# Performance work log

Measured on AMD Instinct MI355X. Metric: run time of the kernel, lower is better.

Reference implementation:

```python
import jax, jax.numpy as jnp
import numpy as np

B, S, NH, HID, NL = 64, 512, 16, 512, 16
W_WIN, PAD, THR, BW = 5, 2, 5.0, 0.1
D_IN = 1 + 2 * NH


def setup_inputs():
    key = jax.random.key(0)
    ks = jax.random.split(key, 16)
    time = jax.random.uniform(ks[0], (B, S)) * 1000.0
    mag = 15.0 + jax.random.normal(ks[1], (B, S))
    err = 0.01 + 0.1 * jax.random.uniform(ks[2], (B, S))
    sc = 0.05
    p = {}
    p["light_curve"] = jnp.stack([time, mag, err], axis=1)  # (B,3,S)
    p["valid_mask"] = jnp.ones((B, S), dtype=bool)
    p["frequency"] = 0.5 + 4.5 * jax.random.uniform(ks[3], (B,))
    p["W_ih0"] = sc * jax.random.normal(ks[4], (3 * HID, D_IN))
    p["b_ih0"] = jnp.zeros((3 * HID,))
    p["W_hh0"] = sc * jax.random.normal(ks[5], (3 * HID, HID))
    p["b_hh0"] = jnp.zeros((3 * HID,))
    p["W_ih1"] = sc * jax.random.normal(ks[6], (3 * HID, HID))
    p["b_ih1"] = jnp.zeros((3 * HID,))
    p["W_hh1"] = sc * jax.random.normal(ks[7], (3 * HID, HID))
    p["b_hh1"] = jnp.zeros((3 * HID,))
    p["Wl1"] = sc * jax.random.normal(ks[8], (HID, HID))
    p["bl1"] = jnp.zeros((HID,))
    p["Wl2"] = sc * jax.random.normal(ks[9], (NL, HID))
    p["bl2"] = jnp.zeros((NL,))
    return p


def _flag_outliers(phase, mag):
    # Sorted-window weighted (Epanechnikov in circular phase-delta) mean/std outlier test.
    # Caller guarantees all points valid (setup uses an all-True mask), so index_select == identity.
    perm = jnp.argsort(phase)
    ps, ms = phase[perm], mag[perm]

    def windows(x):
        xp = jnp.concatenate([x[-PAD:], x, x[:PAD]])  # circular pad
        return jnp.stack([xp[i:i + S] for i in range(W_WIN)], axis=-1)  # (S, w)

    wp, wm = windows(ps), windows(ms)
    cols = jnp.array([i for i in range(W_WIN) if i != PAD])
    dphi = wp[:, cols] - wp[:, PAD:PAD + 1]
    dphi = jnp.remainder(dphi - 0.5, 1.0) - 0.5
    wgt = 0.75 * (1.0 - dphi ** 2)
    wmm = wm[:, cols]
    wsum = wgt.sum(-1)
    loc = (wmm * wgt).sum(-1) / wsum
    scale = jnp.sqrt((((wmm - loc[:, None]) ** 2) * wgt).sum(-1) / (wsum - 1.0))
    thr = loc + THR * scale
    sigma = jnp.zeros_like(mag).at[perm].set(thr)  # inverse-permute (index_copy_)
    return mag > sigma


def _gru_layer(x, W_ih, b_ih, W_hh, b_hh):
    # torch nn.GRU cell math; x: (B,S,D) -> (B,S,H)
    xW = jnp.einsum('bsd,gd->bsg', x, W_ih) + b_ih  # (B,S,3H)

    def step(h, xt):
        hW = h @ W_hh.T + b_hh
        xr, xz, xn = jnp.split(xt, 3, axis=-1)
        hr, hz, hn = jnp.split(hW, 3, axis=-1)
        r = jax.nn.sigmoid(xr + hr)
        z = jax.nn.sigmoid(xz + hz)
        n = jnp.tanh(xn + r * hn)
        h = (1.0 - z) * n + z * h
        return h, h

    h0 = jnp.zeros((x.shape[0], W_hh.shape[1]), x.dtype)
    _, hs = jax.lax.scan(step, h0, jnp.swapaxes(xW, 0, 1))
    return jnp.swapaxes(hs, 0, 1)


def reference(light_curve, valid_mask, frequency, W_ih0, b_ih0, W_hh0, b_hh0,
              W_ih1, b_ih1, W_hh1, b_hh1, Wl1, bl1, Wl2, bl2):
    time, mag, err = light_curve[:, 0], light_curve[:, 1], light_curve[:, 2]
    period = 2.0 / frequency[:, None]  # fold_with_double_period=True (default)
    phase = jnp.remainder(time, period) / period
    outlier = jax.vmap(_flag_outliers)(phase, mag)
    is_valid = valid_mask & ~outlier

    # periodic-kernel interpolation on 50-point grid; align phase to brightness max
    grid = jnp.linspace(0.0, 1.0, 50)
    delta = grid[None, :, None] - phase[:, None, :]  # (B,50,S)
    K = jnp.exp((jnp.cos(2.0 * jnp.pi * delta) - 1.0) / BW ** 2)
    Wk = is_valid[:, None, :].astype(K.dtype) * K
    Wk = Wk / Wk.sum(-1, keepdims=True)
    smooth = (Wk * mag[:, None, :]).sum(-1)  # (B,50)
    phase = phase - grid[jnp.argmax(smooth, axis=-1)][:, None]

    # sort by phase, invalid points last; scaler=None -> loc 0, scale 1
    big = jnp.finfo(jnp.float32).max
    idx = jnp.argsort(jnp.where(is_valid, phase, big), axis=-1)
    phase = jnp.take_along_axis(phase, idx, -1)
    mag = jnp.take_along_axis(mag, idx, -1)
    is_valid = jnp.take_along_axis(is_valid, idx, -1)

    # Fourier phase embedding [cos_1..cos_H, sin_1..sin_H] + mag -> (B,S,2H+1)
    k = jnp.arange(1, NH + 1, dtype=phase.dtype)
    ang = 2.0 * jnp.pi * phase[:, :, None] * k
    emb = jnp.concatenate([jnp.cos(ang), jnp.sin(ang), mag[:, :, None]], axis=-1)

    ht = _gru_layer(emb, W_ih0, b_ih0, W_hh0, b_hh0)
    ht = _gru_layer(ht, W_ih1, b_ih1, W_hh1, b_hh1)

    m = is_valid[:, :, None].astype(ht.dtype)  # context='average'
    ctx = (ht * m).sum(1) / m.sum(1)
    h1 = jax.nn.gelu(ctx @ Wl1.T + bl1, approximate=False)
    z = h1 @ Wl2.T + bl2
    return z
```

## Files before the change

### kernel.cpp

```cpp
#include <hip/hip_runtime.h>


typedef unsigned short u16;
typedef unsigned int u32;
typedef unsigned long long u64;

__device__ __forceinline__ float b2f(u16 u) { return __uint_as_float(((u32)u) << 16); }
__device__ __forceinline__ float blo(u32 u) { return __uint_as_float(u << 16); }
__device__ __forceinline__ float bhi(u32 u) { return __uint_as_float(u & 0xffff0000u); }
__device__ __forceinline__ u16 f2b(float f) {
    u32 x = __float_as_uint(f);
    u32 r = x + 0x7fffu + ((x >> 16) & 1u);
    return (u16)(r >> 16);
}

#define SS 512
#define TWO_PI 6.28318530717958647692f
#define BIGF 3.402823466e+38f
#define PANEL_ELEMS (1536 * 512)
#define FLAGS_BYTES 32768
#define FL(g, f) (((g) * 16 + (f)) * 16)
#define F_A 0
#define F_B 2
#define F_C 4
#define G_A 6
#define G_B 8
#define G_C 10
#define F_PRE 12
#define F_CTX 14

struct P {
    const void* lc;
    const void* freq;
    const void* W[12];
    void* out;
    void* ws;
    unsigned long long ws_size;
};

__device__ __forceinline__ bool inputs_are_bf16(const void* freq) {
    const u16* q = (const u16*)freq;
    bool ok = true;
    for (int i = 0; i < 64; ++i) {
        float v = b2f(q[i]);
        ok = ok && (v >= 0.4f) && (v <= 5.5f);
    }
    return ok;
}

template<bool BF>
__device__ __forceinline__ float ldw(const void* p, size_t i) {
    if constexpr (BF) return b2f(((const u16*)p)[i]);
    else              return ((const float*)p)[i];
}
template<bool BF>
__device__ __forceinline__ const void* rowp(const void* base, int row) {
    if constexpr (BF) return (const void*)((const u16*)base + (size_t)row * 512);
    else              return (const void*)((const float*)base + (size_t)row * 512);
}

__device__ __forceinline__ void sc_store_f(float* ptr, float v) {
    __hip_atomic_store(ptr, v, __ATOMIC_RELAXED, __HIP_MEMORY_SCOPE_AGENT);
}
__device__ __forceinline__ float sc_load_f(const float* ptr) {
    return __hip_atomic_load(ptr, __ATOMIC_RELAXED, __HIP_MEMORY_SCOPE_AGENT);
}
__device__ __forceinline__ void sc_store_i(int* ptr, int v) {
    __hip_atomic_store(ptr, v, __ATOMIC_RELAXED, __HIP_MEMORY_SCOPE_AGENT);
}
__device__ __forceinline__ int sc_load_i(const int* ptr) {
    return __hip_atomic_load(ptr, __ATOMIC_RELAXED, __HIP_MEMORY_SCOPE_AGENT);
}
__device__ __forceinline__ void waitge(const int* f, int v, int* dead) {
    if (*dead) return;
    int it = 0;
    while (sc_load_i(f) < v) {
        __builtin_amdgcn_s_sleep(1);
        if (++it > 2000000) { *dead = 1; break; }
    }
}

template<bool BF>
__device__ void build_panel_one(const void* W, int tid, char* panbase) {
    if constexpr (BF) {
        const uint4* Ws = (const uint4*)W;
        uint4* panel = (uint4*)panbase;
        for (int i = tid; i < 1536 * 64; i += 512) {
            int r = i >> 6, k8 = i & 63;
            panel[(size_t)k8 * 1536 + r] = Ws[i];
        }
    } else {
        const float4* Ws = (const float4*)W;
        float4* panel = (float4*)panbase;
        for (int i = tid; i < 1536 * 128; i += 512) {
            int r = i >> 7, k4 = i & 127;
            panel[(size_t)k4 * 1536 + r] = Ws[i];
        }
    }
}
template<bool BF>
__device__ void build_piece(const void* W, int half, int tid, char* panbase) {
    if constexpr (BF) {
        const uint4* Ws = (const uint4*)W;
        uint4* panel = (uint4*)panbase;
        for (int i = tid; i < 768 * 64; i += 512) {
            int r768 = i >> 6, k8 = i & 63;
            int g3 = r768 >> 8, r = r768 & 255;
            int srcrow = g3 * 512 + half * 256 + r;
            panel[(size_t)k8 * 768 + r768] = Ws[(size_t)srcrow * 64 + k8];
        }
    } else {
        const float4* Ws = (const float4*)W;
        float4* panel = (float4*)panbase;
        for (int i = tid; i < 768 * 128; i += 512) {
            int r768 = i >> 7, k4 = i & 127;
            int g3 = r768 >> 8, r = r768 & 255;
            int srcrow = g3 * 512 + half * 256 + r;
            panel[(size_t)k4 * 768 + r768] = Ws[(size_t)srcrow * 128 + k4];
        }
    }
}

template<bool BF>
__device__ __forceinline__ void tridot_panel(const void* panel, int j,
                                             const float* __restrict__ sh,
                                             float& ar, float& az, float& an) {
    if constexpr (BF) {
        const uint4* pr = (const uint4*)panel + j;
        const uint4* pz = pr + 512;
        const uint4* pn = pr + 1024;
        for (int k0 = 0; k0 < 512; k0 += 8) {
            size_t o = (size_t)(k0 >> 3) * 1536;
            float4 h0 = *(const float4*)&sh[k0];
            float4 h1 = *(const float4*)&sh[k0 + 4];
            uint4 a = pr[o], c = pz[o], d = pn[o];
            ar += blo(a.x) * h0.x + bhi(a.x) * h0.y + blo(a.y) * h0.z + bhi(a.y) * h0.w
                + blo(a.z) * h1.x + bhi(a.z) * h1.y + blo(a.w) * h1.z + bhi(a.w) * h1.w;
            az += blo(c.x) * h0.x + bhi(c.x) * h0.y + blo(c.y) * h0.z + bhi(c.y) * h0.w
                + blo(c.z) * h1.x + bhi(c.z) * h1.y + blo(c.w) * h1.z + bhi(c.w) * h1.w;
            an += blo(d.x) * h0.x + bhi(d.x) * h0.y + blo(d.y) * h0.z + bhi(d.y) * h0.w
                + blo(d.z) * h1.x + bhi(d.z) * h1.y + blo(d.w) * h1.z + bhi(d.w) * h1.w;
        }
    } else {
        const float4* pr = (const float4*)panel + j;
        const float4* pz = pr + 512;
        const float4* pn = pr + 1024;
        for (int k0 = 0; k0 < 512; k0 += 8) {
            size_t o = (size_t)(k0 >> 2) * 1536;
            float4 h0 = *(const float4*)&sh[k0];
            float4 h1 = *(const float4*)&sh[k0 + 4];
            float4 a0 = pr[o], a1 = pr[o + 1536];
            float4 c0 = pz[o], c1 = pz[o + 1536];
            float4 d0 = pn[o], d1 = pn[o + 1536];
            ar += a0.x * h0.x + a0.y * h0.y + a0.z * h0.z + a0.w * h0.w
                + a1.x * h1.x + a1.y * h1.y + a1.z * h1.z + a1.w * h1.w;
            az += c0.x * h0.x + c0.y * h0.y + c0.z * h0.z + c0.w * h0.w
                + c1.x * h1.x + c1.y * h1.y + c1.z * h1.z + c1.w * h1.w;
            an += d0.x * h0.x + d0.y * h0.y + d0.z * h0.z + d0.w * h0.w
                + d1.x * h1.x + d1.y * h1.y + d1.z * h1.z + d1.w * h1.w;
        }
    }
}

template<bool BF>
__device__ __forceinline__ void tridot_piece(const void* panel, int r,
                                             const float* __restrict__ sh,
                                             float& ar, float& az, float& an) {
    if constexpr (BF) {
        const uint4* pr = (const uint4*)panel + r;
        const uint4* pz = pr + 256;
        const uint4* pn = pr + 512;
        for (int k0 = 0; k0 < 512; k0 += 8) {
            size_t o = (size_t)(k0 >> 3) * 768;
            float4 h0 = *(const float4*)&sh[k0];
            float4 h1 = *(const float4*)&sh[k0 + 4];
            uint4 a = pr[o], c = pz[o], d = pn[o];
            ar += blo(a.x) * h0.x + bhi(a.x) * h0.y + blo(a.y) * h0.z + bhi(a.y) * h0.w
                + blo(a.z) * h1.x + bhi(a.z) * h1.y + blo(a.w) * h1.z + bhi(a.w) * h1.w;
            az += blo(c.x) * h0.x + bhi(c.x) * h0.y + blo(c.y) * h0.z + bhi(c.y) * h0.w
                + blo(c.z) * h1.x + bhi(c.z) * h1.y + blo(c.w) * h1.z + bhi(c.w) * h1.w;
            an += blo(d.x) * h0.x + bhi(d.x) * h0.y + blo(d.y) * h0.z + bhi(d.y) * h0.w
                + blo(d.z) * h1.x + bhi(d.z) * h1.y + blo(d.w) * h1.z + bhi(d.w) * h1.w;
        }
    } else {
        const float4* pr = (const float4*)panel + r;
        const float4* pz = pr + 256;
        const float4* pn = pr + 512;
        for (int k0 = 0; k0 < 512; k0 += 8) {
            size_t o = (size_t)(k0 >> 2) * 768;
            float4 h0 = *(const float4*)&sh[k0];
            float4 h1 = *(const float4*)&sh[k0 + 4];
            float4 a0 = pr[o], a1 = pr[o + 768];
            float4 c0 = pz[o], c1 = pz[o + 768];
            float4 d0 = pn[o], d1 = pn[o + 768];
            ar += a0.x * h0.x + a0.y * h0.y + a0.z * h0.z + a0.w * h0.w
                + a1.x * h1.x + a1.y * h1.y + a1.z * h1.z + a1.w * h1.w;
            az += c0.x * h0.x + c0.y * h0.y + c0.z * h0.z + c0.w * h0.w
                + c1.x * h1.x + c1.y * h1.y + c1.z * h1.z + c1.w * h1.w;
            an += d0.x * h0.x + d0.y * h0.y + d0.z * h0.z + d0.w * h0.w
                + d1.x * h1.x + d1.y * h1.y + d1.z * h1.z + d1.w * h1.w;
        }
    }
}

template<bool BF>
__device__ __forceinline__ float dot512(const void* vr, const float* __restrict__ sh) {
    float acc = 0.f;
    if constexpr (BF) {
        const u32* pr = (const u32*)vr;
        for (int k0 = 0; k0 < 512; k0 += 8) {
            float4 h0 = *(const float4*)&sh[k0];
            float4 h1 = *(const float4*)&sh[k0 + 4];
            uint4 a = *(const uint4*)(pr + (k0 >> 1));
            acc += blo(a.x) * h0.x + bhi(a.x) * h0.y + blo(a.y) * h0.z + bhi(a.y) * h0.w
                 + blo(a.z) * h1.x + bhi(a.z) * h1.y + blo(a.w) * h1.z + bhi(a.w) * h1.w;
        }
    } else {
        const float* pr = (const float*)vr;
        for (int k0 = 0; k0 < 512; k0 += 8) {
            float4 h0 = *(const float4*)&sh[k0];
            float4 h1 = *(const float4*)&sh[k0 + 4];
            float4 a0 = *(const float4*)(pr + k0), a1 = *(const float4*)(pr + k0 + 4);
            acc += a0.x * h0.x + a0.y * h0.y + a0.z * h0.z + a0.w * h0.w
                 + a1.x * h1.x + a1.y * h1.y + a1.z * h1.z + a1.w * h1.w;
        }
    }
    return acc;
}

struct PreShm {
    float ph[512], mg[512], skey[512], sig[512], vld[512];
    int   sidx[512];
    float ps2[512], ms2[512], vs2[512];
    float pn[50][8], pd[50][8], smoothv[50];
    float gshift, nv;
};

__device__ void bitonic512(float* skey, int* sidx, int tid) {
    for (int k = 2; k <= 512; k <<= 1) {
        for (int j = k >> 1; j > 0; j >>= 1) {
            int ixj = tid ^ j;
            if (ixj > tid) {
                float ka = skey[tid], kb = skey[ixj];
                int ia = sidx[tid], ib = sidx[ixj];
                bool up = ((tid & k) == 0);
                bool agtb = (ka > kb) || (ka == kb && ia > ib);
                if (agtb == up) {
                    skey[tid] = kb; skey[ixj] = ka;
                    sidx[tid] = ib; sidx[ixj] = ia;
                }
            }
            __syncthreads();
        }
    }
}

template<bool BF>
__device__ void preproc_core(const P& p, PreShm& s, int b, int tid) {
    float period = 2.0f / ldw<BF>(p.freq, b);
    float t = ldw<BF>(p.lc, (size_t)b * 3 * SS + tid);
    float m = ldw<BF>(p.lc, (size_t)b * 3 * SS + SS + tid);
    float ph0 = fmodf(t, period) / period;
    s.ph[tid] = ph0; s.mg[tid] = m;
    s.skey[tid] = ph0; s.sidx[tid] = tid;
    __syncthreads();
    bitonic512(s.skey, s.sidx, tid);
    {
        float pc = s.skey[tid];
        float wv[4], mv[4];
        float wsum = 0.f, wm = 0.f;
        const int offs[4] = {-2, -1, 1, 2};
#pragma unroll
        for (int c = 0; c < 4; ++c) {
            int jj = (tid + offs[c]) & 511;
            float d = s.skey[jj] - pc;
            float u = d - 0.5f; u = u - floorf(u);
            float dphi = u - 0.5f;
            float w = 0.75f * (1.0f - dphi * dphi);
            float mm = s.mg[s.sidx[jj]];
            wv[c] = w; mv[c] = mm;
            wsum += w; wm += w * mm;
        }
        float loc = wm / wsum;
        float s2 = 0.f;
#pragma unroll
        for (int c = 0; c < 4; ++c) { float dm = mv[c] - loc; s2 += dm * dm * wv[c]; }
        float scale = sqrtf(s2 / (wsum - 1.0f));
        s.sig[s.sidx[tid]] = loc + 5.0f * scale;
    }
    __syncthreads();
    s.vld[tid] = (s.mg[tid] > s.sig[tid]) ? 0.0f : 1.0f;
    __syncthreads();
    if (tid == 0) {
        float acc = 0.f;
        for (int i = 0; i < 512; ++i) acc += s.vld[i];
        s.nv = acc;
    }
    {
        int g = tid >> 3, pq = tid & 7;
        if (g < 50) {
            float gv = (float)g * (1.0f / 49.0f);
            float num = 0.f, den = 0.f;
            int s0 = pq * 64;
            for (int ss = s0; ss < s0 + 64; ++ss) {
                float d = gv - s.ph[ss];
                float c = cosf(TWO_PI * d);
                float K = expf((c - 1.0f) * 100.0f);
                float w = s.vld[ss] * K;
                den += w; num += w * s.mg[ss];
            }
            s.pn[g][pq] = num; s.pd[g][pq] = den;
        }
    }
    __syncthreads();
    if (tid < 50) {
        float num = 0.f, den = 0.f;
#pragma unroll
        for (int c = 0; c < 8; ++c) { num += s.pn[tid][c]; den += s.pd[tid][c]; }
        s.smoothv[tid] = num / den;
    }
    __syncthreads();
    if (tid == 0) {
        float best = s.smoothv[0]; int bi = 0;
        for (int g = 1; g < 50; ++g) if (s.smoothv[g] > best) { best = s.smoothv[g]; bi = g; }
        s.gshift = (float)bi * (1.0f / 49.0f);
    }
    __syncthreads();
    float p2 = s.ph[tid] - s.gshift;
    s.ph[tid] = p2;
    s.skey[tid] = (s.vld[tid] > 0.f) ? p2 : BIGF;
    s.sidx[tid] = tid;
    __syncthreads();
    bitonic512(s.skey, s.sidx, tid);
    {
        int o = s.sidx[tid];
        s.ps2[tid] = s.ph[o]; s.ms2[tid] = s.mg[o]; s.vs2[tid] = s.vld[o];
    }
    __syncthreads();
}

struct ShmA { PreShm pre; float psb[2][512], msb[2][512]; float h0L[1024]; float eL[2][34]; };
struct ShmB { float h0loc[1024]; };
struct ShmC { float h1L[1024]; float vs2L[2][512]; float nvL[2]; float ctxL[512], gL[512]; };
struct ShmOldA { PreShm pre; float h0[512], h1[512], eL[34]; };
struct ShmU {
    union { ShmA a; ShmB b; ShmC c; ShmOldA o; } u;
    int dead;
};

template<bool BF, bool PAN>
__device__ void run_all(const P& p, ShmU& S) {
    PreShm& pre = S.u.o.pre;
    float* h0 = S.u.o.h0;
    float* h1 = S.u.o.h1;
    float* eL = S.u.o.eL;
    int b = blockIdx.x, tid = threadIdx.x;
    char* panbase = (char*)p.ws + FLAGS_BYTES;
    const size_t PMAT = (size_t)PANEL_ELEMS * (BF ? 2 : 4);

    if constexpr (PAN) {
        build_panel_one<BF>(p.W[2], tid, panbase);
        build_panel_one<BF>(p.W[4], tid, panbase + PMAT);
        build_panel_one<BF>(p.W[6], tid, panbase + 2 * PMAT);
        __threadfence();
    }
    preproc_core<BF>(p, pre, b, tid);

    int j = tid;
    float wr0[33], wz0[33], wn0[33];
#pragma unroll
    for (int d = 0; d < 33; ++d) {
        wr0[d] = ldw<BF>(p.W[0], (size_t)j * 33 + d);
        wz0[d] = ldw<BF>(p.W[0], ((size_t)j + 512) * 33 + d);
        wn0[d] = ldw<BF>(p.W[0], ((size_t)j + 1024) * 33 + d);
    }
    float bi0r = ldw<BF>(p.W[1], j), bi0z = ldw<BF>(p.W[1], j + 512), bi0n = ldw<BF>(p.W[1], j + 1024);
    float bh0r = ldw<BF>(p.W[3], j), bh0z = ldw<BF>(p.W[3], j + 512), bh0n = ldw<BF>(p.W[3], j + 1024);
    float bi1r = ldw<BF>(p.W[5], j), bi1z = ldw<BF>(p.W[5], j + 512), bi1n = ldw<BF>(p.W[5], j + 1024);
    float bh1r = ldw<BF>(p.W[7], j), bh1z = ldw<BF>(p.W[7], j + 512), bh1n = ldw<BF>(p.W[7], j + 1024);

    const void* pan0  = (const void*)panbase;
    const void* pan1x = (const void*)(panbase + PMAT);
    const void* pan1h = (const void*)(panbase + 2 * PMAT);
    const void *w0r = rowp<BF>(p.W[2], j), *w0z = rowp<BF>(p.W[2], j + 512), *w0n = rowp<BF>(p.W[2], j + 1024);
    const void *x1r = rowp<BF>(p.W[4], j), *x1z = rowp<BF>(p.W[4], j + 512), *x1n = rowp<BF>(p.W[4], j + 1024);
    const void *w1r = rowp<BF>(p.W[6], j), *w1z = rowp<BF>(p.W[6], j + 512), *w1n = rowp<BF>(p.W[6], j + 1024);

    h0[j] = 0.f; h1[j] = 0.f;
    float cacc = 0.f;
    __syncthreads();

    for (int tt = 0; tt < 512; ++tt) {
        if (j < 16) {
            float ang = TWO_PI * pre.ps2[tt] * (float)(j + 1);
            float sv, cv; sincosf(ang, &sv, &cv);
            eL[j] = cv; eL[16 + j] = sv;
        }
        if (j == 32) eL[32] = pre.ms2[tt];
        __syncthreads();
        float xr = bi0r, xz = bi0z, xn = bi0n;
#pragma unroll
        for (int d = 0; d < 33; ++d) {
            float e = eL[d];
            xr += wr0[d] * e; xz += wz0[d] * e; xn += wn0[d] * e;
        }
        float ar = bh0r, az = bh0z, an = bh0n;
        if constexpr (PAN) tridot_panel<BF>(pan0, j, h0, ar, az, an);
        else {
            for (int k = 0; k < 512; ++k) {
                float h = h0[k];
                ar += ldw<BF>(w0r, k) * h; az += ldw<BF>(w0z, k) * h; an += ldw<BF>(w0n, k) * h;
            }
        }
        float h0prev = h0[j];
        float r0 = 1.0f / (1.0f + expf(-(xr + ar)));
        float z0 = 1.0f / (1.0f + expf(-(xz + az)));
        float n0 = tanhf(xn + r0 * an);
        float nh0 = (1.0f - z0) * n0 + z0 * h0prev;
        __syncthreads();
        h0[j] = nh0;
        __syncthreads();
        float yr = bi1r, yz = bi1z, yn = bi1n;
        float cr = bh1r, cz = bh1z, cn = bh1n;
        if constexpr (PAN) {
            tridot_panel<BF>(pan1x, j, h0, yr, yz, yn);
            tridot_panel<BF>(pan1h, j, h1, cr, cz, cn);
        } else {
            for (int k = 0; k < 512; ++k) {
                float h = h0[k], g = h1[k];
                yr += ldw<BF>(x1r, k) * h; yz += ldw<BF>(x1z, k) * h; yn += ldw<BF>(x1n, k) * h;
                cr += ldw<BF>(w1r, k) * g; cz += ldw<BF>(w1z, k) * g; cn += ldw<BF>(w1n, k) * g;
            }
        }
        float h1prev = h1[j];
        float r1 = 1.0f / (1.0f + expf(-(yr + cr)));
        float z1 = 1.0f / (1.0f + expf(-(yz + cz)));
        float n1 = tanhf(yn + r1 * cn);
        float nh1 = (1.0f - z1) * n1 + z1 * h1prev;
        cacc += pre.vs2[tt] * nh1;
        __syncthreads();
        h1[j] = nh1;
    }
    __syncthreads();

    h0[j] = cacc / pre.nv;
    __syncthreads();
    float a1 = ldw<BF>(p.W[9], j) + dot512<BF>(rowp<BF>(p.W[8], j), h0);
    float g = 0.5f * a1 * (1.0f + erff(a1 * 0.70710678118654752440f));
    __syncthreads();
    h1[j] = g;
    __syncthreads();
    if (j < 16) {
        float a2 = ldw<BF>(p.W[11], j) + dot512<BF>(rowp<BF>(p.W[10], j), h1);
        if constexpr (BF) ((u16*)p.out)[(size_t)b * 16 + j] = f2b(a2);
        else              ((float*)p.out)[(size_t)b * 16 + j] = a2;
    }
}

__global__ __launch_bounds__(512) void fused_kernel_old(P p) {
    __shared__ ShmU S;
    bool bf = inputs_are_bf16(p.freq);
    u64 PMAT = bf ? 1572864ull : 3145728ull;
    bool pan = (p.ws && p.ws_size >= (u64)FLAGS_BYTES + 3 * PMAT);
    if (bf) { if (pan) run_all<true, true>(p, S);  else run_all<true, false>(p, S); }
    else    { if (pan) run_all<false, true>(p, S); else run_all<false, false>(p, S); }
}


template<bool BF>
__device__ void runA(const P& p, ShmU& S, int g, int hf, int tid, char* pan,
                     float* h0r, float* pp, int* flags) {
    build_piece<BF>(p.W[2], hf, tid, pan);
    __threadfence();
    int myb = 2 * g + hf, ob = 2 * g + (1 - hf);
    preproc_core<BF>(p, S.u.a.pre, myb, tid);
    sc_store_f(&pp[(size_t)myb * 2048 + tid], S.u.a.pre.ps2[tid]);
    sc_store_f(&pp[(size_t)myb * 2048 + 512 + tid], S.u.a.pre.ms2[tid]);
    sc_store_f(&pp[(size_t)myb * 2048 + 1024 + tid], S.u.a.pre.vs2[tid]);
    if (tid == 0) sc_store_f(&pp[(size_t)myb * 2048 + 1536], S.u.a.pre.nv);
    asm volatile("s_waitcnt vmcnt(0)" ::: "memory");
    __syncthreads();
    if (tid == 0) sc_store_i(&flags[FL(g, F_PRE + hf)], 1);
    S.u.a.psb[hf][tid] = S.u.a.pre.ps2[tid];
    S.u.a.msb[hf][tid] = S.u.a.pre.ms2[tid];
    if (tid == 0) waitge(&flags[FL(g, F_PRE + (1 - hf))], 1, &S.dead);
    __syncthreads();
    S.u.a.psb[1 - hf][tid] = sc_load_f(&pp[(size_t)ob * 2048 + tid]);
    S.u.a.msb[1 - hf][tid] = sc_load_f(&pp[(size_t)ob * 2048 + 512 + tid]);

    const int r = tid & 255, bb = tid >> 8;
    const int j = hf * 256 + r;
    float wr0[33], wz0[33], wn0[33];
#pragma unroll
    for (int d = 0; d < 33; ++d) {
        wr0[d] = ldw<BF>(p.W[0], (size_t)j * 33 + d);
        wz0[d] = ldw<BF>(p.W[0], ((size_t)j + 512) * 33 + d);
        wn0[d] = ldw<BF>(p.W[0], ((size_t)j + 1024) * 33 + d);
    }
    float bi0r = ldw<BF>(p.W[1], j), bi0z = ldw<BF>(p.W[1], j + 512), bi0n = ldw<BF>(p.W[1], j + 1024);
    float bh0r = ldw<BF>(p.W[3], j), bh0z = ldw<BF>(p.W[3], j + 512), bh0n = ldw<BF>(p.W[3], j + 1024);

    S.u.a.h0L[tid] = 0.f; S.u.a.h0L[tid + 512] = 0.f;
    __syncthreads();

    for (int t = 0; t < 512; ++t) {
        if (t > 0) {
            if (tid == 0) waitge(&flags[FL(g, F_A + (1 - hf))], t, &S.dead);
            __syncthreads();
            S.u.a.h0L[bb * 512 + (1 - hf) * 256 + r] =
                sc_load_f(&h0r[(size_t)g * 2048 + ((t - 1) & 1) * 1024 + (1 - hf) * 512 + bb * 256 + r]);
            __syncthreads();
            if (tid == 0) sc_store_i(&flags[FL(g, G_A + hf)], t);
        }
        if (tid < 16) {
            float ang = TWO_PI * S.u.a.psb[0][t] * (float)(tid + 1);
            float sv, cv; sincosf(ang, &sv, &cv);
            S.u.a.eL[0][tid] = cv; S.u.a.eL[0][16 + tid] = sv;
        } else if (tid < 32) {
            int k = tid - 16;
            float ang = TWO_PI * S.u.a.psb[1][t] * (float)(k + 1);
            float sv, cv; sincosf(ang, &sv, &cv);
            S.u.a.eL[1][k] = cv; S.u.a.eL[1][16 + k] = sv;
        }
        if (tid == 32) S.u.a.eL[0][32] = S.u.a.msb[0][t];
        if (tid == 33) S.u.a.eL[1][32] = S.u.a.msb[1][t];
        __syncthreads();
        float xr = bi0r, xz = bi0z, xn = bi0n;
#pragma unroll
        for (int d = 0; d < 33; ++d) {
            float e = S.u.a.eL[bb][d];
            xr += wr0[d] * e; xz += wz0[d] * e; xn += wn0[d] * e;
        }
        float ar = bh0r, az = bh0z, an = bh0n;
        tridot_piece<BF>(pan, r, &S.u.a.h0L[bb * 512], ar, az, an);
        float h0prev = S.u.a.h0L[bb * 512 + j];
        float r0 = 1.0f / (1.0f + expf(-(xr + ar)));
        float z0 = 1.0f / (1.0f + expf(-(xz + az)));
        float n0 = tanhf(xn + r0 * an);
        float nh0 = (1.0f - z0) * n0 + z0 * h0prev;
        __syncthreads();
        S.u.a.h0L[bb * 512 + j] = nh0;
        if (tid == 0 && t >= 2) {
            waitge(&flags[FL(g, G_A + (1 - hf))], t - 1, &S.dead);
            waitge(&flags[FL(g, G_B + 0)], t - 1, &S.dead);
            waitge(&flags[FL(g, G_B + 1)], t - 1, &S.dead);
        }
        __syncthreads();
        sc_store_f(&h0r[(size_t)g * 2048 + (t & 1) * 1024 + hf * 512 + bb * 256 + r], nh0);
        asm volatile("s_waitcnt vmcnt(0)" ::: "memory");
        __syncthreads();
        if (tid == 0) sc_store_i(&flags[FL(g, F_A + hf)], t + 1);
    }
}

template<bool BF>
__device__ void runB(const P& p, ShmU& S, int g, int hf, int tid, char* pan,
                     float* h0r, float* yrng, int* flags) {
    build_piece<BF>(p.W[4], hf, tid, pan);
    __threadfence();
    __syncthreads();
    const int r = tid & 255, bb = tid >> 8;
    const int j = hf * 256 + r;
    float bi1r = ldw<BF>(p.W[5], j), bi1z = ldw<BF>(p.W[5], j + 512), bi1n = ldw<BF>(p.W[5], j + 1024);

    for (int t = 0; t < 512; ++t) {
        if (tid == 0) {
            waitge(&flags[FL(g, F_A + 0)], t + 1, &S.dead);
            waitge(&flags[FL(g, F_A + 1)], t + 1, &S.dead);
        }
        __syncthreads();
        S.u.b.h0loc[bb * 512 + r] =
            sc_load_f(&h0r[(size_t)g * 2048 + (t & 1) * 1024 + 0 * 512 + bb * 256 + r]);
        S.u.b.h0loc[bb * 512 + 256 + r] =
            sc_load_f(&h0r[(size_t)g * 2048 + (t & 1) * 1024 + 1 * 512 + bb * 256 + r]);
        __syncthreads();
        if (tid == 0) sc_store_i(&flags[FL(g, G_B + hf)], t + 1);
        float yr = bi1r, yz = bi1z, yn = bi1n;
        tridot_piece<BF>(pan, r, &S.u.b.h0loc[bb * 512], yr, yz, yn);
        if (tid == 0 && t >= 2) waitge(&flags[FL(g, G_C + hf)], t - 1, &S.dead);
        __syncthreads();
        float* slot = &yrng[(size_t)g * 6144 + (t & 1) * 3072 + hf * 1536];
        sc_store_f(&slot[bb * 256 + r], yr);
        sc_store_f(&slot[512 + bb * 256 + r], yz);
        sc_store_f(&slot[1024 + bb * 256 + r], yn);
        asm volatile("s_waitcnt vmcnt(0)" ::: "memory");
        __syncthreads();
        if (tid == 0) sc_store_i(&flags[FL(g, F_B + hf)], t + 1);
    }
}

template<bool BF>
__device__ void runC(const P& p, ShmU& S, int g, int hf, int tid, char* pan,
                     float* yrng, float* h1r, float* pp, float* ctxb, int* flags) {
    build_piece<BF>(p.W[6], hf, tid, pan);
    __threadfence();
    if (tid == 0) {
        waitge(&flags[FL(g, F_PRE + 0)], 1, &S.dead);
        waitge(&flags[FL(g, F_PRE + 1)], 1, &S.dead);
    }
    __syncthreads();
    S.u.c.vs2L[0][tid] = sc_load_f(&pp[(size_t)(2 * g) * 2048 + 1024 + tid]);
    S.u.c.vs2L[1][tid] = sc_load_f(&pp[(size_t)(2 * g + 1) * 2048 + 1024 + tid]);
    if (tid == 0) {
        S.u.c.nvL[0] = sc_load_f(&pp[(size_t)(2 * g) * 2048 + 1536]);
        S.u.c.nvL[1] = sc_load_f(&pp[(size_t)(2 * g + 1) * 2048 + 1536]);
    }
    S.u.c.h1L[tid] = 0.f; S.u.c.h1L[tid + 512] = 0.f;
    __syncthreads();

    const int r = tid & 255, bb = tid >> 8;
    const int j = hf * 256 + r;
    float bh1r = ldw<BF>(p.W[7], j), bh1z = ldw<BF>(p.W[7], j + 512), bh1n = ldw<BF>(p.W[7], j + 1024);
    float cacc = 0.f;

    for (int t = 0; t < 512; ++t) {
        if (tid == 0) {
            waitge(&flags[FL(g, F_B + hf)], t + 1, &S.dead);
            if (t > 0) waitge(&flags[FL(g, F_C + (1 - hf))], t, &S.dead);
        }
        __syncthreads();
        if (t > 0) {
            S.u.c.h1L[bb * 512 + (1 - hf) * 256 + r] =
                sc_load_f(&h1r[(size_t)g * 2048 + ((t - 1) & 1) * 1024 + (1 - hf) * 512 + bb * 256 + r]);
        }
        const float* slot = &yrng[(size_t)g * 6144 + (t & 1) * 3072 + hf * 1536];
        float yr = sc_load_f(&slot[bb * 256 + r]);
        float yz = sc_load_f(&slot[512 + bb * 256 + r]);
        float yn = sc_load_f(&slot[1024 + bb * 256 + r]);
        __syncthreads();
        if (tid == 0) sc_store_i(&flags[FL(g, G_C + hf)], t + 1);
        float cr = bh1r, cz = bh1z, cn = bh1n;
        tridot_piece<BF>(pan, r, &S.u.c.h1L[bb * 512], cr, cz, cn);
        float h1prev = S.u.c.h1L[bb * 512 + j];
        float r1 = 1.0f / (1.0f + expf(-(yr + cr)));
        float z1 = 1.0f / (1.0f + expf(-(yz + cz)));
        float n1 = tanhf(yn + r1 * cn);
        float nh1 = (1.0f - z1) * n1 + z1 * h1prev;
        cacc += S.u.c.vs2L[bb][t] * nh1;
        __syncthreads();
        S.u.c.h1L[bb * 512 + j] = nh1;
        if (tid == 0 && t >= 2) waitge(&flags[FL(g, G_C + (1 - hf))], t - 1, &S.dead);
        __syncthreads();
        sc_store_f(&h1r[(size_t)g * 2048 + (t & 1) * 1024 + hf * 512 + bb * 256 + r], nh1);
        asm volatile("s_waitcnt vmcnt(0)" ::: "memory");
        __syncthreads();
        if (tid == 0) sc_store_i(&flags[FL(g, F_C + hf)], t + 1);
    }

    sc_store_f(&ctxb[(size_t)g * 1024 + hf * 512 + bb * 256 + r], cacc);
    asm volatile("s_waitcnt vmcnt(0)" ::: "memory");
    __syncthreads();
    if (tid == 0) {
        sc_store_i(&flags[FL(g, F_CTX + hf)], 1);
        waitge(&flags[FL(g, F_CTX + (1 - hf))], 1, &S.dead);
    }
    __syncthreads();
    float nv = S.u.c.nvL[hf];
    S.u.c.ctxL[tid] = sc_load_f(&ctxb[(size_t)g * 1024 + (tid >> 8) * 512 + hf * 256 + (tid & 255)]) / nv;
    __syncthreads();
    float a1 = ldw<BF>(p.W[9], tid) + dot512<BF>(rowp<BF>(p.W[8], tid), S.u.c.ctxL);
    float gg = 0.5f * a1 * (1.0f + erff(a1 * 0.70710678118654752440f));
    __syncthreads();
    S.u.c.gL[tid] = gg;
    __syncthreads();
    if (tid < 16) {
        float a2 = ldw<BF>(p.W[11], tid) + dot512<BF>(rowp<BF>(p.W[10], tid), S.u.c.gL);
        int hb = 2 * g + hf;
        if constexpr (BF) ((u16*)p.out)[(size_t)hb * 16 + tid] = f2b(a2);
        else              ((float*)p.out)[(size_t)hb * 16 + tid] = a2;
    }
}

template<bool BF>
__device__ void run_pipe(const P& p, ShmU& S) {
    const int bid = blockIdx.x;
    const int piece = bid & 7;
    if (piece >= 6) return;
    const int g = bid >> 3;
    const int role = piece >> 1, hf = piece & 1;
    const int tid = threadIdx.x;
    if (tid == 0) S.dead = 0;
    __syncthreads();

    char* wsb = (char*)p.ws;
    int* flags = (int*)wsb;
    const size_t PIECE = BF ? 786432 : 1572864;
    char* pans = wsb + FLAGS_BYTES;
    char* mypan = pans + (size_t)piece * PIECE;
    float* h0r  = (float*)(pans + 6 * PIECE);
    float* yrng = h0r + (size_t)32 * 2048;
    float* h1r  = yrng + (size_t)32 * 6144;
    float* pp   = h1r + (size_t)32 * 2048;
    float* ctxb = pp + (size_t)64 * 2048;

    if (role == 0)      runA<BF>(p, S, g, hf, tid, mypan, h0r, pp, flags);
    else if (role == 1) runB<BF>(p, S, g, hf, tid, mypan, h0r, yrng, flags);
    else                runC<BF>(p, S, g, hf, tid, mypan, yrng, h1r, pp, ctxb, flags);
}

__global__ __launch_bounds__(512) void fused_kernel_pipe(P p) {
    __shared__ ShmU S;
    if (inputs_are_bf16(p.freq)) run_pipe<true>(p, S);
    else                         run_pipe<false>(p, S);
}

extern "C" void kernel_launch(void* const* d_in, const int* in_sizes, int n_in,
                              void* d_out, int out_size, void* d_ws, size_t ws_size,
                              hipStream_t stream) {
    P p;
    p.lc = d_in[0];
    p.freq = d_in[2];
    for (int i = 0; i < 12; ++i) p.W[i] = d_in[3 + i];
    p.out = d_out;
    p.ws = d_ws;
    p.ws_size = (unsigned long long)ws_size;

    const size_t need_pipe = 11436032ull;
    if (d_ws && ws_size >= need_pipe) {
        hipMemsetAsync(d_ws, 0, FLAGS_BYTES, stream);
        fused_kernel_pipe<<<256, 512, 0, stream>>>(p);
    } else {
        fused_kernel_old<<<64, 512, 0, stream>>>(p);
    }
    (void)in_sizes; (void)n_in; (void)out_size;
}
```

Baseline: 14.31 ms.

## Split GRU pipeline hidden dimension across four blocks per group instead of two

Each group of the layer-pipelined GRU now handles four batch rows and splits the 512 hidden units across four blocks per role (128 rows each) rather than two halves. The change is meant to halve the per-block weight panel read each timestep and shorten the serial recurrent dot product. In exchange it adds more cross-block flag handshakes and hidden-state exchange through global memory at every step. The launch still uses 256 blocks, so 192 blocks do work versus 192 before, but each group now covers four batch rows with a finer hidden split.

Measured after the change: 17.89 ms. 25.0% more time.

```diff
diff --git a/kernel.cpp b/kernel.cpp
--- a/kernel.cpp
+++ b/kernel.cpp
@@ -18,16 +18,17 @@
 #define TWO_PI 6.28318530717958647692f
 #define BIGF 3.402823466e+38f
 #define PANEL_ELEMS (1536 * 512)
-#define FLAGS_BYTES 32768
-#define FL(g, f) (((g) * 16 + (f)) * 16)
-#define F_A 0
-#define F_B 2
-#define F_C 4
-#define G_A 6
-#define G_B 8
-#define G_C 10
-#define F_PRE 12
-#define F_CTX 14
+#define FLAGS_BYTES 65536
+#define FL(g, f) (((g) * 64 + (f)) * 16)
+#define F_A   0
+#define G_A   4
+#define F_B   8
+#define G_B   12
+#define F_C   16
+#define G_CH  20
+#define G_C   24
+#define F_PRE 28
+#define F_CTX 32
 
 struct P {
     const void* lc;
@@ -99,24 +100,24 @@
     }
 }
 template<bool BF>
-__device__ void build_piece(const void* W, int half, int tid, char* panbase) {
+__device__ void build_piece(const void* W, int q, int tid, char* panbase) {
     if constexpr (BF) {
         const uint4* Ws = (const uint4*)W;
         uint4* panel = (uint4*)panbase;
-        for (int i = tid; i < 768 * 64; i += 512) {
-            int r768 = i >> 6, k8 = i & 63;
-            int g3 = r768 >> 8, r = r768 & 255;
-            int srcrow = g3 * 512 + half * 256 + r;
-            panel[(size_t)k8 * 768 + r768] = Ws[(size_t)srcrow * 64 + k8];
+        for (int i = tid; i < 384 * 64; i += 512) {
+            int r384 = i >> 6, k8 = i & 63;
+            int g3 = r384 >> 7, r = r384 & 127;
+            int srcrow = g3 * 512 + q * 128 + r;
+            panel[(size_t)k8 * 384 + r384] = Ws[(size_t)srcrow * 64 + k8];
         }
     } else {
         const float4* Ws = (const float4*)W;
         float4* panel = (float4*)panbase;
-        for (int i = tid; i < 768 * 128; i += 512) {
-            int r768 = i >> 7, k4 = i & 127;
-            int g3 = r768 >> 8, r = r768 & 255;
-            int srcrow = g3 * 512 + half * 256 + r;
-            panel[(size_t)k4 * 768 + r768] = Ws[(size_t)srcrow * 128 + k4];
+        for (int i = tid; i < 384 * 128; i += 512) {
+            int r384 = i >> 7, k4 = i & 127;
+            int g3 = r384 >> 7, r = r384 & 127;
+            int srcrow = g3 * 512 + q * 128 + r;
+            panel[(size_t)k4 * 384 + r384] = Ws[(size_t)srcrow * 128 + k4];
         }
     }
 }
@@ -163,15 +164,15 @@
 }
 
 template<bool BF>
-__device__ __forceinline__ void tridot_piece(const void* panel, int r,
-                                             const float* __restrict__ sh,
-                                             float& ar, float& az, float& an) {
+__device__ __forceinline__ void tridot_q(const void* panel, int r,
+                                         const float* __restrict__ sh,
+                                         float& ar, float& az, float& an) {
     if constexpr (BF) {
         const uint4* pr = (const uint4*)panel + r;
-        const uint4* pz = pr + 256;
-        const uint4* pn = pr + 512;
+        const uint4* pz = pr + 128;
+        const uint4* pn = pr + 256;
         for (int k0 = 0; k0 < 512; k0 += 8) {
-            size_t o = (size_t)(k0 >> 3) * 768;
+            size_t o = (size_t)(k0 >> 3) * 384;
             float4 h0 = *(const float4*)&sh[k0];
             float4 h1 = *(const float4*)&sh[k0 + 4];
             uint4 a = pr[o], c = pz[o], d = pn[o];
@@ -184,15 +185,15 @@
         }
     } else {
         const float4* pr = (const float4*)panel + r;
-        const float4* pz = pr + 256;
-        const float4* pn = pr + 512;
+        const float4* pz = pr + 128;
+        const float4* pn = pr + 256;
         for (int k0 = 0; k0 < 512; k0 += 8) {
-            size_t o = (size_t)(k0 >> 2) * 768;
+            size_t o = (size_t)(k0 >> 2) * 384;
             float4 h0 = *(const float4*)&sh[k0];
             float4 h1 = *(const float4*)&sh[k0 + 4];
-            float4 a0 = pr[o], a1 = pr[o + 768];
-            float4 c0 = pz[o], c1 = pz[o + 768];
-            float4 d0 = pn[o], d1 = pn[o + 768];
+            float4 a0 = pr[o], a1 = pr[o + 384];
+            float4 c0 = pz[o], c1 = pz[o + 384];
+            float4 d0 = pn[o], d1 = pn[o + 384];
             ar += a0.x * h0.x + a0.y * h0.y + a0.z * h0.z + a0.w * h0.w
                 + a1.x * h1.x + a1.y * h1.y + a1.z * h1.z + a1.w * h1.w;
             az += c0.x * h0.x + c0.y * h0.y + c0.z * h0.z + c0.w * h0.w
@@ -339,9 +340,9 @@
     __syncthreads();
 }
 
-struct ShmA { PreShm pre; float psb[2][512], msb[2][512]; float h0L[1024]; float eL[2][34]; };
-struct ShmB { float h0loc[1024]; };
-struct ShmC { float h1L[1024]; float vs2L[2][512]; float nvL[2]; float ctxL[512], gL[512]; };
+struct ShmA { PreShm pre; float psb[4][512], msb[4][512]; float h0L[2048]; float eL[4][34]; };
+struct ShmB { float h0loc[2048]; };
+struct ShmC { float h1L[2048]; float vs2L[4][512]; float nvL[4]; float ctxL[512], gL[512]; };
 struct ShmOldA { PreShm pre; float h0[512], h1[512], eL[34]; };
 struct ShmU {
     union { ShmA a; ShmB b; ShmC c; ShmOldA o; } u;
@@ -468,11 +469,12 @@
 
 
 template<bool BF>
-__device__ void runA(const P& p, ShmU& S, int g, int hf, int tid, char* pan,
+__device__ void runA(const P& p, ShmU& S, int g, int q, int tid, char* pan,
                      float* h0r, float* pp, int* flags) {
-    build_piece<BF>(p.W[2], hf, tid, pan);
+    int* dead = &S.dead;
+    build_piece<BF>(p.W[2], q, tid, pan);
     __threadfence();
-    int myb = 2 * g + hf, ob = 2 * g + (1 - hf);
+    int myb = 4 * g + q;
     preproc_core<BF>(p, S.u.a.pre, myb, tid);
     sc_store_f(&pp[(size_t)myb * 2048 + tid], S.u.a.pre.ps2[tid]);
     sc_store_f(&pp[(size_t)myb * 2048 + 512 + tid], S.u.a.pre.ms2[tid]);
@@ -480,16 +482,20 @@
     if (tid == 0) sc_store_f(&pp[(size_t)myb * 2048 + 1536], S.u.a.pre.nv);
     asm volatile("s_waitcnt vmcnt(0)" ::: "memory");
     __syncthreads();
-    if (tid == 0) sc_store_i(&flags[FL(g, F_PRE + hf)], 1);
-    S.u.a.psb[hf][tid] = S.u.a.pre.ps2[tid];
-    S.u.a.msb[hf][tid] = S.u.a.pre.ms2[tid];
-    if (tid == 0) waitge(&flags[FL(g, F_PRE + (1 - hf))], 1, &S.dead);
-    __syncthreads();
-    S.u.a.psb[1 - hf][tid] = sc_load_f(&pp[(size_t)ob * 2048 + tid]);
-    S.u.a.msb[1 - hf][tid] = sc_load_f(&pp[(size_t)ob * 2048 + 512 + tid]);
-
-    const int r = tid & 255, bb = tid >> 8;
-    const int j = hf * 256 + r;
+    if (tid == 0) sc_store_i(&flags[FL(g, F_PRE + q)], 1);
+    S.u.a.psb[q][tid] = S.u.a.pre.ps2[tid];
+    S.u.a.msb[q][tid] = S.u.a.pre.ms2[tid];
+    if (tid < 4 && tid != q) waitge(&flags[FL(g, F_PRE + tid)], 1, dead);
+    __syncthreads();
+#pragma unroll
+    for (int qq = 0; qq < 4; ++qq) {
+        if (qq == q) continue;
+        S.u.a.psb[qq][tid] = sc_load_f(&pp[(size_t)(4 * g + qq) * 2048 + tid]);
+        S.u.a.msb[qq][tid] = sc_load_f(&pp[(size_t)(4 * g + qq) * 2048 + 512 + tid]);
+    }
+
+    const int r = tid & 127, bb = tid >> 7;
+    const int j = q * 128 + r;
     float wr0[33], wz0[33], wn0[33];
 #pragma unroll
     for (int d = 0; d < 33; ++d) {
@@ -500,30 +506,31 @@
     float bi0r = ldw<BF>(p.W[1], j), bi0z = ldw<BF>(p.W[1], j + 512), bi0n = ldw<BF>(p.W[1], j + 1024);
     float bh0r = ldw<BF>(p.W[3], j), bh0z = ldw<BF>(p.W[3], j + 512), bh0n = ldw<BF>(p.W[3], j + 1024);
 
-    S.u.a.h0L[tid] = 0.f; S.u.a.h0L[tid + 512] = 0.f;
+    float* h0L = S.u.a.h0L;
+    for (int i = tid; i < 2048; i += 512) h0L[i] = 0.f;
     __syncthreads();
 
     for (int t = 0; t < 512; ++t) {
         if (t > 0) {
-            if (tid == 0) waitge(&flags[FL(g, F_A + (1 - hf))], t, &S.dead);
+            if (tid < 4 && tid != q) waitge(&flags[FL(g, F_A + tid)], t, dead);
             __syncthreads();
-            S.u.a.h0L[bb * 512 + (1 - hf) * 256 + r] =
-                sc_load_f(&h0r[(size_t)g * 2048 + ((t - 1) & 1) * 1024 + (1 - hf) * 512 + bb * 256 + r]);
+            const float* src = &h0r[(size_t)((g * 2 + ((t - 1) & 1)) * 4 + bb) * 512];
+#pragma unroll
+            for (int qq = 0; qq < 4; ++qq) {
+                if (qq == q) continue;
+                h0L[bb * 512 + qq * 128 + r] = sc_load_f(&src[qq * 128 + r]);
+            }
             __syncthreads();
-            if (tid == 0) sc_store_i(&flags[FL(g, G_A + hf)], t);
-        }
-        if (tid < 16) {
-            float ang = TWO_PI * S.u.a.psb[0][t] * (float)(tid + 1);
+            if (tid == 0) sc_store_i(&flags[FL(g, G_A + q)], t);
+        }
+        if (tid < 64) {
+            int bq = tid >> 4, k = tid & 15;
+            float ang = TWO_PI * S.u.a.psb[bq][t] * (float)(k + 1);
             float sv, cv; sincosf(ang, &sv, &cv);
-            S.u.a.eL[0][tid] = cv; S.u.a.eL[0][16 + tid] = sv;
-        } else if (tid < 32) {
-            int k = tid - 16;
-            float ang = TWO_PI * S.u.a.psb[1][t] * (float)(k + 1);
-            float sv, cv; sincosf(ang, &sv, &cv);
-            S.u.a.eL[1][k] = cv; S.u.a.eL[1][16 + k] = sv;
-        }
-        if (tid == 32) S.u.a.eL[0][32] = S.u.a.msb[0][t];
-        if (tid == 33) S.u.a.eL[1][32] = S.u.a.msb[1][t];
+            S.u.a.eL[bq][k] = cv; S.u.a.eL[bq][16 + k] = sv;
+        } else if (tid < 68) {
+            S.u.a.eL[tid - 64][32] = S.u.a.msb[tid - 64][t];
+        }
         __syncthreads();
         float xr = bi0r, xz = bi0z, xn = bi0n;
 #pragma unroll
@@ -532,131 +539,129 @@
             xr += wr0[d] * e; xz += wz0[d] * e; xn += wn0[d] * e;
         }
         float ar = bh0r, az = bh0z, an = bh0n;
-        tridot_piece<BF>(pan, r, &S.u.a.h0L[bb * 512], ar, az, an);
-        float h0prev = S.u.a.h0L[bb * 512 + j];
+        tridot_q<BF>(pan, r, &h0L[bb * 512], ar, az, an);
+        float h0prev = h0L[bb * 512 + j];
         float r0 = 1.0f / (1.0f + expf(-(xr + ar)));
         float z0 = 1.0f / (1.0f + expf(-(xz + az)));
         float n0 = tanhf(xn + r0 * an);
         float nh0 = (1.0f - z0) * n0 + z0 * h0prev;
         __syncthreads();
-        S.u.a.h0L[bb * 512 + j] = nh0;
-        if (tid == 0 && t >= 2) {
-            waitge(&flags[FL(g, G_A + (1 - hf))], t - 1, &S.dead);
-            waitge(&flags[FL(g, G_B + 0)], t - 1, &S.dead);
-            waitge(&flags[FL(g, G_B + 1)], t - 1, &S.dead);
-        }
-        __syncthreads();
-        sc_store_f(&h0r[(size_t)g * 2048 + (t & 1) * 1024 + hf * 512 + bb * 256 + r], nh0);
+        h0L[bb * 512 + j] = nh0;
+        if (t >= 2) {
+            if (tid < 4 && tid != q) waitge(&flags[FL(g, G_A + tid)], t - 1, dead);
+            if (tid >= 4 && tid < 8) waitge(&flags[FL(g, G_B + tid - 4)], t - 1, dead);
+        }
+        __syncthreads();
+        sc_store_f(&h0r[(size_t)((g * 2 + (t & 1)) * 4 + bb) * 512 + j], nh0);
         asm volatile("s_waitcnt vmcnt(0)" ::: "memory");
         __syncthreads();
-        if (tid == 0) sc_store_i(&flags[FL(g, F_A + hf)], t + 1);
-    }
-}
-
-template<bool BF>
-__device__ void runB(const P& p, ShmU& S, int g, int hf, int tid, char* pan,
+        if (tid == 0) sc_store_i(&flags[FL(g, F_A + q)], t + 1);
+    }
+}
+
+template<bool BF>
+__device__ void runB(const P& p, ShmU& S, int g, int q, int tid, char* pan,
                      float* h0r, float* yrng, int* flags) {
-    build_piece<BF>(p.W[4], hf, tid, pan);
+    int* dead = &S.dead;
+    build_piece<BF>(p.W[4], q, tid, pan);
     __threadfence();
     __syncthreads();
-    const int r = tid & 255, bb = tid >> 8;
-    const int j = hf * 256 + r;
+    const int r = tid & 127, bb = tid >> 7;
+    const int j = q * 128 + r;
     float bi1r = ldw<BF>(p.W[5], j), bi1z = ldw<BF>(p.W[5], j + 512), bi1n = ldw<BF>(p.W[5], j + 1024);
+    float* h0loc = S.u.b.h0loc;
 
     for (int t = 0; t < 512; ++t) {
-        if (tid == 0) {
-            waitge(&flags[FL(g, F_A + 0)], t + 1, &S.dead);
-            waitge(&flags[FL(g, F_A + 1)], t + 1, &S.dead);
-        }
-        __syncthreads();
-        S.u.b.h0loc[bb * 512 + r] =
-            sc_load_f(&h0r[(size_t)g * 2048 + (t & 1) * 1024 + 0 * 512 + bb * 256 + r]);
-        S.u.b.h0loc[bb * 512 + 256 + r] =
-            sc_load_f(&h0r[(size_t)g * 2048 + (t & 1) * 1024 + 1 * 512 + bb * 256 + r]);
-        __syncthreads();
-        if (tid == 0) sc_store_i(&flags[FL(g, G_B + hf)], t + 1);
+        if (tid < 4) waitge(&flags[FL(g, F_A + tid)], t + 1, dead);
+        __syncthreads();
+        const float* src = &h0r[(size_t)((g * 2 + (t & 1)) * 4 + bb) * 512];
+#pragma unroll
+        for (int qq = 0; qq < 4; ++qq)
+            h0loc[bb * 512 + qq * 128 + r] = sc_load_f(&src[qq * 128 + r]);
+        __syncthreads();
+        if (tid == 0) sc_store_i(&flags[FL(g, G_B + q)], t + 1);
         float yr = bi1r, yz = bi1z, yn = bi1n;
-        tridot_piece<BF>(pan, r, &S.u.b.h0loc[bb * 512], yr, yz, yn);
-        if (tid == 0 && t >= 2) waitge(&flags[FL(g, G_C + hf)], t - 1, &S.dead);
-        __syncthreads();
-        float* slot = &yrng[(size_t)g * 6144 + (t & 1) * 3072 + hf * 1536];
-        sc_store_f(&slot[bb * 256 + r], yr);
-        sc_store_f(&slot[512 + bb * 256 + r], yz);
-        sc_store_f(&slot[1024 + bb * 256 + r], yn);
+        tridot_q<BF>(pan, r, &h0loc[bb * 512], yr, yz, yn);
+        if (tid == 0 && t >= 2) waitge(&flags[FL(g, G_C + q)], t - 1, dead);
+        __syncthreads();
+        float* slot = &yrng[(size_t)((g * 2 + (t & 1)) * 4 + q) * 1536];
+        sc_store_f(&slot[bb * 128 + r], yr);
+        sc_store_f(&slot[512 + bb * 128 + r], yz);
+        sc_store_f(&slot[1024 + bb * 128 + r], yn);
         asm volatile("s_waitcnt vmcnt(0)" ::: "memory");
         __syncthreads();
-        if (tid == 0) sc_store_i(&flags[FL(g, F_B + hf)], t + 1);
-    }
-}
-
-template<bool BF>
-__device__ void runC(const P& p, ShmU& S, int g, int hf, int tid, char* pan,
+        if (tid == 0) sc_store_i(&flags[FL(g, F_B + q)], t + 1);
+    }
+}
+
+template<bool BF>
+__device__ void runC(const P& p, ShmU& S, int g, int q, int tid, char* pan,
                      float* yrng, float* h1r, float* pp, float* ctxb, int* flags) {
-    build_piece<BF>(p.W[6], hf, tid, pan);
+    int* dead = &S.dead;
+    build_piece<BF>(p.W[6], q, tid, pan);
     __threadfence();
-    if (tid == 0) {
-        waitge(&flags[FL(g, F_PRE + 0)], 1, &S.dead);
-        waitge(&flags[FL(g, F_PRE + 1)], 1, &S.dead);
-    }
-    __syncthreads();
-    S.u.c.vs2L[0][tid] = sc_load_f(&pp[(size_t)(2 * g) * 2048 + 1024 + tid]);
-    S.u.c.vs2L[1][tid] = sc_load_f(&pp[(size_t)(2 * g + 1) * 2048 + 1024 + tid]);
-    if (tid == 0) {
-        S.u.c.nvL[0] = sc_load_f(&pp[(size_t)(2 * g) * 2048 + 1536]);
-        S.u.c.nvL[1] = sc_load_f(&pp[(size_t)(2 * g + 1) * 2048 + 1536]);
-    }
-    S.u.c.h1L[tid] = 0.f; S.u.c.h1L[tid + 512] = 0.f;
-    __syncthreads();
-
-    const int r = tid & 255, bb = tid >> 8;
-    const int j = hf * 256 + r;
+    if (tid < 4) waitge(&flags[FL(g, F_PRE + tid)], 1, dead);
+    __syncthreads();
+#pragma unroll
+    for (int qq = 0; qq < 4; ++qq)
+        S.u.c.vs2L[qq][tid] = sc_load_f(&pp[(size_t)(4 * g + qq) * 2048 + 1024 + tid]);
+    if (tid < 4) S.u.c.nvL[tid] = sc_load_f(&pp[(size_t)(4 * g + tid) * 2048 + 1536]);
+    float* h1L = S.u.c.h1L;
+    for (int i = tid; i < 2048; i += 512) h1L[i] = 0.f;
+    __syncthreads();
+
+    const int r = tid & 127, bb = tid >> 7;
+    const int j = q * 128 + r;
     float bh1r = ldw<BF>(p.W[7], j), bh1z = ldw<BF>(p.W[7], j + 512), bh1n = ldw<BF>(p.W[7], j + 1024);
     float cacc = 0.f;
 
     for (int t = 0; t < 512; ++t) {
+        if (tid == 4) waitge(&flags[FL(g, F_B + q)], t + 1, dead);
+        if (t > 0 && tid < 4 && tid != q) waitge(&flags[FL(g, F_C + tid)], t, dead);
+        __syncthreads();
+        if (t > 0) {
+            const float* src = &h1r[(size_t)((g * 2 + ((t - 1) & 1)) * 4 + bb) * 512];
+#pragma unroll
+            for (int qq = 0; qq < 4; ++qq) {
+                if (qq == q) continue;
+                h1L[bb * 512 + qq * 128 + r] = sc_load_f(&src[qq * 128 + r]);
+            }
+        }
+        const float* slot = &yrng[(size_t)((g * 2 + (t & 1)) * 4 + q) * 1536];
+        float yr = sc_load_f(&slot[bb * 128 + r]);
+        float yz = sc_load_f(&slot[512 + bb * 128 + r]);
+        float yn = sc_load_f(&slot[1024 + bb * 128 + r]);
+        __syncthreads();
         if (tid == 0) {
-            waitge(&flags[FL(g, F_B + hf)], t + 1, &S.dead);
-            if (t > 0) waitge(&flags[FL(g, F_C + (1 - hf))], t, &S.dead);
-        }
-        __syncthreads();
-        if (t > 0) {
-            S.u.c.h1L[bb * 512 + (1 - hf) * 256 + r] =
-                sc_load_f(&h1r[(size_t)g * 2048 + ((t - 1) & 1) * 1024 + (1 - hf) * 512 + bb * 256 + r]);
-        }
-        const float* slot = &yrng[(size_t)g * 6144 + (t & 1) * 3072 + hf * 1536];
-        float yr = sc_load_f(&slot[bb * 256 + r]);
-        float yz = sc_load_f(&slot[512 + bb * 256 + r]);
-        float yn = sc_load_f(&slot[1024 + bb * 256 + r]);
-        __syncthreads();
-        if (tid == 0) sc_store_i(&flags[FL(g, G_C + hf)], t + 1);
+            sc_store_i(&flags[FL(g, G_C + q)], t + 1);
+            sc_store_i(&flags[FL(g, G_CH + q)], t);
+        }
         float cr = bh1r, cz = bh1z, cn = bh1n;
-        tridot_piece<BF>(pan, r, &S.u.c.h1L[bb * 512], cr, cz, cn);
-        float h1prev = S.u.c.h1L[bb * 512 + j];
+        tridot_q<BF>(pan, r, &h1L[bb * 512], cr, cz, cn);
+        float h1prev = h1L[bb * 512 + j];
         float r1 = 1.0f / (1.0f + expf(-(yr + cr)));
         float z1 = 1.0f / (1.0f + expf(-(yz + cz)));
         float n1 = tanhf(yn + r1 * cn);
         float nh1 = (1.0f - z1) * n1 + z1 * h1prev;
         cacc += S.u.c.vs2L[bb][t] * nh1;
         __syncthreads();
-        S.u.c.h1L[bb * 512 + j] = nh1;
-        if (tid == 0 && t >= 2) waitge(&flags[FL(g, G_C + (1 - hf))], t - 1, &S.dead);
-        __syncthreads();
-        sc_store_f(&h1r[(size_t)g * 2048 + (t & 1) * 1024 + hf * 512 + bb * 256 + r], nh1);
+        h1L[bb * 512 + j] = nh1;
+        if (t >= 2 && tid < 4 && tid != q) waitge(&flags[FL(g, G_CH + tid)], t - 1, dead);
+        __syncthreads();
+        sc_store_f(&h1r[(size_t)((g * 2 + (t & 1)) * 4 + bb) * 512 + j], nh1);
         asm volatile("s_waitcnt vmcnt(0)" ::: "memory");
         __syncthreads();
-        if (tid == 0) sc_store_i(&flags[FL(g, F_C + hf)], t + 1);
-    }
-
-    sc_store_f(&ctxb[(size_t)g * 1024 + hf * 512 + bb * 256 + r], cacc);
+        if (tid == 0) sc_store_i(&flags[FL(g, F_C + q)], t + 1);
+    }
+
+    sc_store_f(&ctxb[(size_t)(g * 4 + bb) * 512 + j], cacc);
     asm volatile("s_waitcnt vmcnt(0)" ::: "memory");
     __syncthreads();
-    if (tid == 0) {
-        sc_store_i(&flags[FL(g, F_CTX + hf)], 1);
-        waitge(&flags[FL(g, F_CTX + (1 - hf))], 1, &S.dead);
-    }
-    __syncthreads();
-    float nv = S.u.c.nvL[hf];
-    S.u.c.ctxL[tid] = sc_load_f(&ctxb[(size_t)g * 1024 + (tid >> 8) * 512 + hf * 256 + (tid & 255)]) / nv;
+    if (tid == 0) sc_store_i(&flags[FL(g, F_CTX + q)], 1);
+    if (tid < 4 && tid != q) waitge(&flags[FL(g, F_CTX + tid)], 1, dead);
+    __syncthreads();
+    float nv = S.u.c.nvL[q];
+    S.u.c.ctxL[tid] = sc_load_f(&ctxb[(size_t)(g * 4 + q) * 512 + tid]) / nv;
     __syncthreads();
     float a1 = ldw<BF>(p.W[9], tid) + dot512<BF>(rowp<BF>(p.W[8], tid), S.u.c.ctxL);
     float gg = 0.5f * a1 * (1.0f + erff(a1 * 0.70710678118654752440f));
@@ -665,7 +670,7 @@
     __syncthreads();
     if (tid < 16) {
         float a2 = ldw<BF>(p.W[11], tid) + dot512<BF>(rowp<BF>(p.W[10], tid), S.u.c.gL);
-        int hb = 2 * g + hf;
+        int hb = 4 * g + q;
         if constexpr (BF) ((u16*)p.out)[(size_t)hb * 16 + tid] = f2b(a2);
         else              ((float*)p.out)[(size_t)hb * 16 + tid] = a2;
     }
@@ -674,28 +679,28 @@
 template<bool BF>
 __device__ void run_pipe(const P& p, ShmU& S) {
     const int bid = blockIdx.x;
-    const int piece = bid & 7;
-    if (piece >= 6) return;
-    const int g = bid >> 3;
-    const int role = piece >> 1, hf = piece & 1;
+    const int piece = bid & 15;
+    if (piece >= 12) return;
+    const int g = bid >> 4;
+    const int role = piece >> 2, q = piece & 3;
     const int tid = threadIdx.x;
     if (tid == 0) S.dead = 0;
     __syncthreads();
 
     char* wsb = (char*)p.ws;
     int* flags = (int*)wsb;
-    const size_t PIECE = BF ? 786432 : 1572864;
+    const size_t PIECE = BF ? 393216 : 786432;
     char* pans = wsb + FLAGS_BYTES;
     char* mypan = pans + (size_t)piece * PIECE;
-    float* h0r  = (float*)(pans + 6 * PIECE);
-    float* yrng = h0r + (size_t)32 * 2048;
-    float* h1r  = yrng + (size_t)32 * 6144;
-    float* pp   = h1r + (size_t)32 * 2048;
-    float* ctxb = pp + (size_t)64 * 2048;
-
-    if (role == 0)      runA<BF>(p, S, g, hf, tid, mypan, h0r, pp, flags);
-    else if (role == 1) runB<BF>(p, S, g, hf, tid, mypan, h0r, yrng, flags);
-    else                runC<BF>(p, S, g, hf, tid, mypan, yrng, h1r, pp, ctxb, flags);
+    float* h0r  = (float*)(pans + 12 * PIECE);
+    float* yrng = h0r + 65536;
+    float* h1r  = yrng + 196608;
+    float* pp   = h1r + 65536;
+    float* ctxb = pp + 131072;
+
+    if (role == 0)      runA<BF>(p, S, g, q, tid, mypan, h0r, pp, flags);
+    else if (role == 1) runB<BF>(p, S, g, q, tid, mypan, h0r, yrng, flags);
+    else                runC<BF>(p, S, g, q, tid, mypan, yrng, h1r, pp, ctxb, flags);
 }
 
 __global__ __launch_bounds__(512) void fused_kernel_pipe(P p) {
@@ -715,7 +720,7 @@
     p.ws = d_ws;
     p.ws_size = (unsigned long long)ws_size;
 
-    const size_t need_pipe = 11436032ull;
+    const size_t need_pipe = 11468800ull;
     if (d_ws && ws_size >= need_pipe) {
         hipMemsetAsync(d_ws, 0, FLAGS_BYTES, stream);
         fused_kernel_pipe<<<256, 512, 0, stream>>>(p);
```
